# Optimization experiments

Measured on AMD Instinct MI355X. Metric: run time of the kernel, lower is better.

## Reference

```python
import jax, jax.numpy as jnp
import numpy as np

EPS = 1e-3  # Keras BatchNormalization default epsilon


def _bn(x, gamma, beta, mean, var):
    # inference batch norm, channels-last
    inv = gamma * jax.lax.rsqrt(var + EPS)
    return x * inv + (beta - mean * inv)


def setup_inputs() -> dict:
    key = jax.random.key(0)
    ks = jax.random.split(key, 13)
    B, D, H, W, C, F = 2, 48, 48, 48, 64, 128
    return {
        "x": jax.random.normal(ks[0], (B, D, H, W, C), dtype=jnp.float32),
        "dw_kernel": jax.random.normal(ks[1], (3, 3, 3, 1, C), dtype=jnp.float32) * 0.1,
        "dw_bias": jax.random.normal(ks[2], (C,), dtype=jnp.float32) * 0.1,
        "bn1_gamma": jax.random.uniform(ks[3], (C,), dtype=jnp.float32, minval=0.5, maxval=1.5),
        "bn1_beta": jax.random.normal(ks[4], (C,), dtype=jnp.float32) * 0.1,
        "bn1_mean": jax.random.normal(ks[5], (C,), dtype=jnp.float32) * 0.1,
        "bn1_var": jax.random.uniform(ks[6], (C,), dtype=jnp.float32, minval=0.5, maxval=1.5),
        "pw_kernel": jax.random.normal(ks[7], (C, F), dtype=jnp.float32) * 0.1,
        "pw_bias": jax.random.normal(ks[8], (F,), dtype=jnp.float32) * 0.1,
        "bn2_gamma": jax.random.uniform(ks[9], (F,), dtype=jnp.float32, minval=0.5, maxval=1.5),
        "bn2_beta": jax.random.normal(ks[10], (F,), dtype=jnp.float32) * 0.1,
        "bn2_mean": jax.random.normal(ks[11], (F,), dtype=jnp.float32) * 0.1,
        "bn2_var": jax.random.uniform(ks[12], (F,), dtype=jnp.float32, minval=0.5, maxval=1.5),
    }


def reference(x, dw_kernel, dw_bias, bn1_gamma, bn1_beta, bn1_mean, bn1_var,
              pw_kernel, pw_bias, bn2_gamma, bn2_beta, bn2_mean, bn2_var):
    C = x.shape[-1]
    # True depthwise conv3d (replaces the per-channel Python loop of Conv3D(1,...))
    y = jax.lax.conv_general_dilated(
        x, dw_kernel,
        window_strides=(1, 1, 1), padding="SAME",
        dimension_numbers=("NDHWC", "DHWIO", "NDHWC"),
        feature_group_count=C,
    ) + dw_bias
    y = jax.nn.relu(_bn(y, bn1_gamma, bn1_beta, bn1_mean, bn1_var))
    # pointwise 1x1x1 conv == channel GEMM
    z = jnp.einsum("bdhwc,cf->bdhwf", y, pw_kernel) + pw_bias
    z = jax.nn.relu(_bn(z, bn2_gamma, bn2_beta, bn2_mean, bn2_var))
    return z
```

## Files before the change

kernel.cpp:

```cpp
#include <hip/hip_runtime.h>
#include <hip/hip_bf16.h>

#define EPS 1e-3f

typedef __attribute__((ext_vector_type(8))) short short8;
typedef __attribute__((ext_vector_type(4))) float v4f;

__device__ __forceinline__ unsigned short f2bf(float f) {
    unsigned int u = __float_as_uint(f);
    unsigned int r = (u + 0x7fffu + ((u >> 16) & 1u)) >> 16;
    return (unsigned short)r;
}

__global__ __launch_bounds__(256) void prep_kernel(
    const float* __restrict__ dwb,
    const float* __restrict__ g1, const float* __restrict__ b1,
    const float* __restrict__ m1, const float* __restrict__ v1,
    const float* __restrict__ pw, const float* __restrict__ pwb,
    const float* __restrict__ g2, const float* __restrict__ b2,
    const float* __restrict__ m2, const float* __restrict__ v2,
    float* __restrict__ scale1, float* __restrict__ shift1,
    float* __restrict__ s2, float* __restrict__ t2,
    unsigned short* __restrict__ Wt)
{
    int tid = threadIdx.x;
    if (blockIdx.x == 0) {
        if (tid < 64) {
            float inv = g1[tid] * rsqrtf(v1[tid] + EPS);
            scale1[tid] = inv;
            shift1[tid] = dwb[tid] * inv + b1[tid] - m1[tid] * inv;
        }
        if (tid < 128) {
            float inv = g2[tid] * rsqrtf(v2[tid] + EPS);
            s2[tid] = inv;
            t2[tid] = pwb[tid] * inv + b2[tid] - m2[tid] * inv;
        }
    }
    int idx = blockIdx.x * 256 + tid;
    int j     = idx & 7;
    int lane  = (idx >> 3) & 63;
    int kstep = (idx >> 9) & 1;
    int ntile = idx >> 10;
    int k = kstep * 32 + (lane >> 4) * 8 + j;
    int f = ntile * 16 + (lane & 15);
    Wt[idx] = f2bf(pw[k * 128 + f]);
}

__global__ __launch_bounds__(256) void fused_kernel(
    const float* __restrict__ x,
    const float* __restrict__ wgt,
    const float* __restrict__ scale1,
    const float* __restrict__ shift1,
    const unsigned short* __restrict__ Wt,
    const float* __restrict__ s2,
    const float* __restrict__ t2,
    float* __restrict__ out)
{
    __shared__ float wS[27 * 64];
    __shared__ float sS[64];
    __shared__ float tS[64];
    __shared__ unsigned short yS[64 * 72];

    int tid = threadIdx.x;
    for (int i = tid; i < 27 * 64; i += 256) wS[i] = wgt[i];
    if (tid < 64) { sS[tid] = scale1[tid]; tS[tid] = shift1[tid]; }
    __syncthreads();

    int n   = blockIdx.x;
    int xcd = n & 7;
    int j   = n >> 3;
    int bd  = xcd * 12 + (j % 12);
    int s   = j / 12;
    int w0  = (s % 3) * 16;
    int h0  = (s / 3) * 4;
    int b   = bd / 48;
    int d   = bd % 48;

    int tx = tid & 15;
    int ty = tid >> 4;
    int c0 = tx * 4;
    int wq = ty & 3;
    int rh = ty >> 2;
    int w0t = w0 + wq * 4;
    int h   = h0 + rh;

    float4 acc[4];
    #pragma unroll
    for (int r = 0; r < 4; ++r) acc[r] = make_float4(0.f, 0.f, 0.f, 0.f);

    float mwL = (w0t >= 1)  ? 1.f : 0.f;
    float mwR = (w0t <= 43) ? 1.f : 0.f;
    int wcl[6];
    #pragma unroll
    for (int p = 0; p < 6; ++p)
        wcl[p] = min(max(w0t - 1 + p, 0), 47) * 64;

    bool hok[3];
    int  hcl[3];
    #pragma unroll
    for (int hh = 0; hh < 3; ++hh) {
        int zh = h + hh - 1;
        hok[hh] = (zh >= 0 && zh < 48);
        hcl[hh] = min(max(zh, 0), 47) * 48 * 64;
    }

    #pragma unroll
    for (int dd = 0; dd < 3; ++dd) {
        int zd = d + dd - 1;
        bool dok = (zd >= 0 && zd < 48);
        int zdc = min(max(zd, 0), 47);
        const float* dp = x + (((long)b * 48 + zdc) * 48 * 48) * 64 + c0;

        float4 xv[3][6];
        #pragma unroll
        for (int hh = 0; hh < 3; ++hh) {
            const float* rowp = dp + hcl[hh];
            #pragma unroll
            for (int p = 0; p < 6; ++p)
                xv[hh][p] = *(const float4*)(rowp + wcl[p]);
        }

        if (dok) {
            #pragma unroll
            for (int hh = 0; hh < 3; ++hh) {
                if (hok[hh]) {
                    xv[hh][0].x *= mwL; xv[hh][0].y *= mwL;
                    xv[hh][0].z *= mwL; xv[hh][0].w *= mwL;
                    xv[hh][5].x *= mwR; xv[hh][5].y *= mwR;
                    xv[hh][5].z *= mwR; xv[hh][5].w *= mwR;
                    #pragma unroll
                    for (int ww = 0; ww < 3; ++ww) {
                        const float4 wv = *(const float4*)(&wS[((dd * 3 + hh) * 3 + ww) * 64 + c0]);
                        #pragma unroll
                        for (int r = 0; r < 4; ++r) {
                            acc[r].x += xv[hh][r + ww].x * wv.x;
                            acc[r].y += xv[hh][r + ww].y * wv.y;
                            acc[r].z += xv[hh][r + ww].z * wv.z;
                            acc[r].w += xv[hh][r + ww].w * wv.w;
                        }
                    }
                }
            }
        }
    }

    {
        float4 s1 = *(const float4*)(&sS[c0]);
        float4 t1 = *(const float4*)(&tS[c0]);
        #pragma unroll
        for (int r = 0; r < 4; ++r) {
            ushort4 o;
            o.x = f2bf(fmaxf(acc[r].x * s1.x + t1.x, 0.f));
            o.y = f2bf(fmaxf(acc[r].y * s1.y + t1.y, 0.f));
            o.z = f2bf(fmaxf(acc[r].z * s1.z + t1.z, 0.f));
            o.w = f2bf(fmaxf(acc[r].w * s1.w + t1.w, 0.f));
            *(ushort4*)(&yS[(ty * 4 + r) * 72 + c0]) = o;
        }
    }
    __syncthreads();

    int wv   = tid >> 6;
    int lane = tid & 63;
    int lrow = lane & 15;
    int quad = lane >> 4;

    const short8 a0 = *(const short8*)(&yS[(wv * 16 + lrow) * 72 + quad * 8]);
    const short8 a1 = *(const short8*)(&yS[(wv * 16 + lrow) * 72 + 32 + quad * 8]);

    v4f g[8];
    #pragma unroll
    for (int nn = 0; nn < 8; ++nn) g[nn] = (v4f){0.f, 0.f, 0.f, 0.f};

    #pragma unroll
    for (int nn = 0; nn < 8; ++nn) {
        short8 b0 = *(const short8*)(Wt + ((nn * 2 + 0) * 64 + lane) * 8);
        short8 b1 = *(const short8*)(Wt + ((nn * 2 + 1) * 64 + lane) * 8);
        g[nn] = __builtin_amdgcn_mfma_f32_16x16x32_bf16(a0, b0, g[nn], 0, 0, 0);
        g[nn] = __builtin_amdgcn_mfma_f32_16x16x32_bf16(a1, b1, g[nn], 0, 0, 0);
    }

    long base_out = ((((long)b * 48 + d) * 48 + (h0 + wv)) * 48 + w0) * 128;
    #pragma unroll
    for (int nn = 0; nn < 8; ++nn) {
        int f = nn * 16 + lrow;
        float sf = s2[f];
        float tf = t2[f];
        #pragma unroll
        for (int r = 0; r < 4; ++r) {
            float v = fmaxf(g[nn][r] * sf + tf, 0.f);
            out[base_out + (quad * 4 + r) * 128 + f] = v;
        }
    }
}

extern "C" void kernel_launch(void* const* d_in, const int* in_sizes, int n_in,
                              void* d_out, int out_size, void* d_ws, size_t ws_size,
                              hipStream_t stream)
{
    const float* x   = (const float*)d_in[0];
    const float* dwk = (const float*)d_in[1];
    const float* dwb = (const float*)d_in[2];
    const float* g1  = (const float*)d_in[3];
    const float* b1  = (const float*)d_in[4];
    const float* m1  = (const float*)d_in[5];
    const float* v1  = (const float*)d_in[6];
    const float* pw  = (const float*)d_in[7];
    const float* pwb = (const float*)d_in[8];
    const float* g2  = (const float*)d_in[9];
    const float* b2  = (const float*)d_in[10];
    const float* m2  = (const float*)d_in[11];
    const float* v2  = (const float*)d_in[12];

    float* outp = (float*)d_out;

    float* scale1 = (float*)d_ws;
    float* shift1 = scale1 + 64;
    float* s2     = scale1 + 128;
    float* t2     = scale1 + 256;
    unsigned short* Wt = (unsigned short*)((char*)d_ws + 2048);

    hipLaunchKernelGGL(prep_kernel, dim3(32), dim3(256), 0, stream,
                       dwb, g1, b1, m1, v1, pw, pwb, g2, b2, m2, v2,
                       scale1, shift1, s2, t2, Wt);

    hipLaunchKernelGGL(fused_kernel, dim3(3456), dim3(256), 0, stream,
                       x, dwk, scale1, shift1, Wt, s2, t2, outp);
}
```

Measured before the change: 211.8 us.

## Compute two depth slices per block to reuse input slabs and weights

Each block now produces two consecutive depth outputs, so it loads four input depth slabs instead of six. Slab loads are interleaved with the FMAs through two register buffers. Pointwise weight fragments and BN2 parameters are loaded once and reused for both slices. Depth and height boundaries are handled by selecting a zeroed weight row instead of branching. Together these cut global traffic and per-block setup, at the cost of higher register pressure, doubled LDS for the bf16 tile, and half as many blocks.

Result: slower. 262.3 us (+23.9%).

```diff
diff --git a/kernel.cpp b/kernel.cpp
--- a/kernel.cpp
+++ b/kernel.cpp
@@ -57,24 +57,26 @@
     float* __restrict__ out)
 {
     __shared__ float wS[27 * 64];
+    __shared__ float wZ[192];
     __shared__ float sS[64];
     __shared__ float tS[64];
-    __shared__ unsigned short yS[64 * 72];
+    __shared__ unsigned short yS[128 * 72];
 
     int tid = threadIdx.x;
     for (int i = tid; i < 27 * 64; i += 256) wS[i] = wgt[i];
+    if (tid < 192) wZ[tid] = 0.f;
     if (tid < 64) { sS[tid] = scale1[tid]; tS[tid] = shift1[tid]; }
     __syncthreads();
 
     int n   = blockIdx.x;
     int xcd = n & 7;
     int j   = n >> 3;
-    int bd  = xcd * 12 + (j % 12);
-    int s   = j / 12;
+    int bd2 = xcd * 6 + (j % 6);
+    int s   = j / 6;
     int w0  = (s % 3) * 16;
     int h0  = (s / 3) * 4;
-    int b   = bd / 48;
-    int d   = bd % 48;
+    int b   = bd2 / 24;
+    int d0  = (bd2 % 24) * 2;
 
     int tx = tid & 15;
     int ty = tid >> 4;
@@ -84,9 +86,12 @@
     int w0t = w0 + wq * 4;
     int h   = h0 + rh;
 
-    float4 acc[4];
-    #pragma unroll
-    for (int r = 0; r < 4; ++r) acc[r] = make_float4(0.f, 0.f, 0.f, 0.f);
+    float4 acc0[4], acc1[4];
+    #pragma unroll
+    for (int r = 0; r < 4; ++r) {
+        acc0[r] = make_float4(0.f, 0.f, 0.f, 0.f);
+        acc1[r] = make_float4(0.f, 0.f, 0.f, 0.f);
+    }
 
     float mwL = (w0t >= 1)  ? 1.f : 0.f;
     float mwR = (w0t <= 43) ? 1.f : 0.f;
@@ -104,57 +109,88 @@
         hcl[hh] = min(max(zh, 0), 47) * 48 * 64;
     }
 
-    #pragma unroll
-    for (int dd = 0; dd < 3; ++dd) {
-        int zd = d + dd - 1;
-        bool dok = (zd >= 0 && zd < 48);
-        int zdc = min(max(zd, 0), 47);
-        const float* dp = x + (((long)b * 48 + zdc) * 48 * 48) * 64 + c0;
-
-        float4 xv[3][6];
+    const float* xb = x + ((long)b * 48) * 147456 + c0;
+
+    auto loadSlab = [&](float4* Xb, int si) {
+        int zdc = min(max(d0 - 1 + si, 0), 47);
+        const float* dp = xb + (long)zdc * 147456;
         #pragma unroll
         for (int hh = 0; hh < 3; ++hh) {
             const float* rowp = dp + hcl[hh];
             #pragma unroll
             for (int p = 0; p < 6; ++p)
-                xv[hh][p] = *(const float4*)(rowp + wcl[p]);
-        }
-
-        if (dok) {
+                Xb[hh * 6 + p] = *(const float4*)(rowp + wcl[p]);
+        }
+    };
+
+    auto fmaOne = [&](const float4* Xb, int dd, float4* accp, bool dok) {
+        #pragma unroll
+        for (int hh = 0; hh < 3; ++hh) {
+            const float* wp = (dok && hok[hh]) ? &wS[(dd * 3 + hh) * 192 + c0]
+                                               : &wZ[c0];
             #pragma unroll
-            for (int hh = 0; hh < 3; ++hh) {
-                if (hok[hh]) {
-                    xv[hh][0].x *= mwL; xv[hh][0].y *= mwL;
-                    xv[hh][0].z *= mwL; xv[hh][0].w *= mwL;
-                    xv[hh][5].x *= mwR; xv[hh][5].y *= mwR;
-                    xv[hh][5].z *= mwR; xv[hh][5].w *= mwR;
-                    #pragma unroll
-                    for (int ww = 0; ww < 3; ++ww) {
-                        const float4 wv = *(const float4*)(&wS[((dd * 3 + hh) * 3 + ww) * 64 + c0]);
-                        #pragma unroll
-                        for (int r = 0; r < 4; ++r) {
-                            acc[r].x += xv[hh][r + ww].x * wv.x;
-                            acc[r].y += xv[hh][r + ww].y * wv.y;
-                            acc[r].z += xv[hh][r + ww].z * wv.z;
-                            acc[r].w += xv[hh][r + ww].w * wv.w;
-                        }
-                    }
+            for (int ww = 0; ww < 3; ++ww) {
+                const float4 wv = *(const float4*)(wp + ww * 64);
+                #pragma unroll
+                for (int r = 0; r < 4; ++r) {
+                    accp[r].x += Xb[hh * 6 + r + ww].x * wv.x;
+                    accp[r].y += Xb[hh * 6 + r + ww].y * wv.y;
+                    accp[r].z += Xb[hh * 6 + r + ww].z * wv.z;
+                    accp[r].w += Xb[hh * 6 + r + ww].w * wv.w;
                 }
             }
         }
-    }
+    };
+
+    auto maskEdges = [&](float4* Xb) {
+        #pragma unroll
+        for (int hh = 0; hh < 3; ++hh) {
+            Xb[hh * 6 + 0].x *= mwL; Xb[hh * 6 + 0].y *= mwL;
+            Xb[hh * 6 + 0].z *= mwL; Xb[hh * 6 + 0].w *= mwL;
+            Xb[hh * 6 + 5].x *= mwR; Xb[hh * 6 + 5].y *= mwR;
+            Xb[hh * 6 + 5].z *= mwR; Xb[hh * 6 + 5].w *= mwR;
+        }
+    };
+
+    bool dv0 = (d0 - 1 >= 0);
+    bool dv3 = (d0 + 2 < 48);
+
+    float4 X[18], Y[18];
+    loadSlab(X, 0);
+    loadSlab(Y, 1);
+
+    maskEdges(X);
+    fmaOne(X, 0, acc0, dv0);
+    loadSlab(X, 2);
+
+    maskEdges(Y);
+    fmaOne(Y, 1, acc0, true);
+    fmaOne(Y, 0, acc1, true);
+    loadSlab(Y, 3);
+
+    maskEdges(X);
+    fmaOne(X, 2, acc0, true);
+    fmaOne(X, 1, acc1, true);
+
+    maskEdges(Y);
+    fmaOne(Y, 2, acc1, dv3);
 
     {
         float4 s1 = *(const float4*)(&sS[c0]);
         float4 t1 = *(const float4*)(&tS[c0]);
         #pragma unroll
         for (int r = 0; r < 4; ++r) {
-            ushort4 o;
-            o.x = f2bf(fmaxf(acc[r].x * s1.x + t1.x, 0.f));
-            o.y = f2bf(fmaxf(acc[r].y * s1.y + t1.y, 0.f));
-            o.z = f2bf(fmaxf(acc[r].z * s1.z + t1.z, 0.f));
-            o.w = f2bf(fmaxf(acc[r].w * s1.w + t1.w, 0.f));
-            *(ushort4*)(&yS[(ty * 4 + r) * 72 + c0]) = o;
+            ushort4 o0, o1;
+            o0.x = f2bf(fmaxf(acc0[r].x * s1.x + t1.x, 0.f));
+            o0.y = f2bf(fmaxf(acc0[r].y * s1.y + t1.y, 0.f));
+            o0.z = f2bf(fmaxf(acc0[r].z * s1.z + t1.z, 0.f));
+            o0.w = f2bf(fmaxf(acc0[r].w * s1.w + t1.w, 0.f));
+            o1.x = f2bf(fmaxf(acc1[r].x * s1.x + t1.x, 0.f));
+            o1.y = f2bf(fmaxf(acc1[r].y * s1.y + t1.y, 0.f));
+            o1.z = f2bf(fmaxf(acc1[r].z * s1.z + t1.z, 0.f));
+            o1.w = f2bf(fmaxf(acc1[r].w * s1.w + t1.w, 0.f));
+            *(ushort4*)(&yS[(ty * 4 + r) * 72 + c0]) = o0;
+            *(ushort4*)(&yS[(64 + ty * 4 + r) * 72 + c0]) = o1;
         }
     }
     __syncthreads();
@@ -164,31 +200,42 @@
     int lrow = lane & 15;
     int quad = lane >> 4;
 
-    const short8 a0 = *(const short8*)(&yS[(wv * 16 + lrow) * 72 + quad * 8]);
-    const short8 a1 = *(const short8*)(&yS[(wv * 16 + lrow) * 72 + 32 + quad * 8]);
-
-    v4f g[8];
-    #pragma unroll
-    for (int nn = 0; nn < 8; ++nn) g[nn] = (v4f){0.f, 0.f, 0.f, 0.f};
-
+    short8 bf0[8], bf1[8];
     #pragma unroll
     for (int nn = 0; nn < 8; ++nn) {
-        short8 b0 = *(const short8*)(Wt + ((nn * 2 + 0) * 64 + lane) * 8);
-        short8 b1 = *(const short8*)(Wt + ((nn * 2 + 1) * 64 + lane) * 8);
-        g[nn] = __builtin_amdgcn_mfma_f32_16x16x32_bf16(a0, b0, g[nn], 0, 0, 0);
-        g[nn] = __builtin_amdgcn_mfma_f32_16x16x32_bf16(a1, b1, g[nn], 0, 0, 0);
-    }
-
-    long base_out = ((((long)b * 48 + d) * 48 + (h0 + wv)) * 48 + w0) * 128;
+        bf0[nn] = *(const short8*)(Wt + ((nn * 2 + 0) * 64 + lane) * 8);
+        bf1[nn] = *(const short8*)(Wt + ((nn * 2 + 1) * 64 + lane) * 8);
+    }
+    float sf[8], tf[8];
     #pragma unroll
     for (int nn = 0; nn < 8; ++nn) {
-        int f = nn * 16 + lrow;
-        float sf = s2[f];
-        float tf = t2[f];
-        #pragma unroll
-        for (int r = 0; r < 4; ++r) {
-            float v = fmaxf(g[nn][r] * sf + tf, 0.f);
-            out[base_out + (quad * 4 + r) * 128 + f] = v;
+        sf[nn] = s2[nn * 16 + lrow];
+        tf[nn] = t2[nn * 16 + lrow];
+    }
+
+    #pragma unroll
+    for (int o = 0; o < 2; ++o) {
+        const short8 a0 = *(const short8*)(&yS[(o * 64 + wv * 16 + lrow) * 72 + quad * 8]);
+        const short8 a1 = *(const short8*)(&yS[(o * 64 + wv * 16 + lrow) * 72 + 32 + quad * 8]);
+
+        v4f g[8];
+        #pragma unroll
+        for (int nn = 0; nn < 8; ++nn) g[nn] = (v4f){0.f, 0.f, 0.f, 0.f};
+        #pragma unroll
+        for (int nn = 0; nn < 8; ++nn) {
+            g[nn] = __builtin_amdgcn_mfma_f32_16x16x32_bf16(a0, bf0[nn], g[nn], 0, 0, 0);
+            g[nn] = __builtin_amdgcn_mfma_f32_16x16x32_bf16(a1, bf1[nn], g[nn], 0, 0, 0);
+        }
+
+        long base_out = ((((long)b * 48 + d0 + o) * 48 + (h0 + wv)) * 48 + w0) * 128;
+        #pragma unroll
+        for (int nn = 0; nn < 8; ++nn) {
+            int f = nn * 16 + lrow;
+            #pragma unroll
+            for (int r = 0; r < 4; ++r) {
+                float v = fmaxf(g[nn][r] * sf[nn] + tf[nn], 0.f);
+                out[base_out + (quad * 4 + r) * 128 + f] = v;
+            }
         }
     }
 }
@@ -223,6 +270,6 @@
                        dwb, g1, b1, m1, v1, pw, pwb, g2, b2, m2, v2,
                        scale1, shift1, s2, t2, Wt);
 
-    hipLaunchKernelGGL(fused_kernel, dim3(3456), dim3(256), 0, stream,
+    hipLaunchKernelGGL(fused_kernel, dim3(1728), dim3(256), 0, stream,
                        x, dwk, scale1, shift1, Wt, s2, t2, outp);
 }
```
